# Kernel optimization log

Hardware: AMD Instinct MI355X
Metric: run time of the kernel (lower is better)

The kernel has to match this reference:

```python
import jax, jax.numpy as jnp
import numpy as np

B, T, D = 1, 2048, 1024
HQ, HKV, HD = 16, 4, 64
G = HQ // HKV
E, TOPK, F = 8, 2, 2752
LB = 0.01
SCALE = HD ** -0.5


def setup_inputs() -> dict:
    key = jax.random.key(0)
    ks = jax.random.split(key, 12)
    s = 0.02
    return {
        "x": jax.random.normal(ks[0], (B, T, D), jnp.float32),
        "g1": jnp.ones((D,), jnp.float32),
        "g2": jnp.ones((D,), jnp.float32),
        "wq": jax.random.normal(ks[1], (D, HQ * HD), jnp.float32) * s,
        "wk": jax.random.normal(ks[2], (D, HKV * HD), jnp.float32) * s,
        "wv": jax.random.normal(ks[3], (D, HKV * HD), jnp.float32) * s,
        "wo": jax.random.normal(ks[4], (D, D), jnp.float32) * s,
        "gate_w": jax.random.normal(ks[5], (D, E), jnp.float32) * s,
        "we_gate": jax.random.normal(ks[6], (E, D, F), jnp.float32) * s,
        "we_up": jax.random.normal(ks[7], (E, D, F), jnp.float32) * s,
        "we_down": jax.random.normal(ks[8], (E, F, D), jnp.float32) * s,
    }


def _rmsnorm(x, g, eps=1e-6):
    return x * g * jax.lax.rsqrt(jnp.mean(x * x, axis=-1, keepdims=True) + eps)


def _rope(q, k):
    # q: [B,HQ,T,HD], k: [B,HKV,T,HD]; standard rotate-half RoPE
    pos = jnp.arange(T, dtype=jnp.float32)
    inv_freq = 1.0 / (10000.0 ** (jnp.arange(0, HD, 2, dtype=jnp.float32) / HD))
    ang = pos[:, None] * inv_freq[None, :]                  # [T, HD/2]
    cos = jnp.concatenate([jnp.cos(ang), jnp.cos(ang)], -1)  # [T, HD]
    sin = jnp.concatenate([jnp.sin(ang), jnp.sin(ang)], -1)

    def rot_half(x):
        x1, x2 = jnp.split(x, 2, axis=-1)
        return jnp.concatenate([-x2, x1], axis=-1)

    def apply(x):
        return x * cos + rot_half(x) * sin
    return apply(q), apply(k)


def _attention(x, g1, wq, wk, wv, wo):
    h = _rmsnorm(x, g1)
    q = (h @ wq).reshape(B, T, HQ, HD).transpose(0, 2, 1, 3)   # [B,HQ,T,HD]
    k = (h @ wk).reshape(B, T, HKV, HD).transpose(0, 2, 1, 3)  # [B,HKV,T,HD]
    v = (h @ wv).reshape(B, T, HKV, HD).transpose(0, 2, 1, 3)
    q, k = _rope(q, k)
    qg = q.reshape(B, HKV, G, T, HD)
    # grouped scores without materializing repeated K/V
    scores = jnp.einsum('bkgtd,bksd->bkgts', qg, k) * SCALE     # [B,HKV,G,T,T]
    causal = jnp.tril(jnp.ones((T, T), bool))
    scores = jnp.where(causal, scores, jnp.float32(-jnp.inf))
    w = jax.nn.softmax(scores, axis=-1)
    o = jnp.einsum('bkgts,bksd->bkgtd', w, v)                  # [B,HKV,G,T,HD]
    o = o.reshape(B, HQ, T, HD).transpose(0, 2, 1, 3).reshape(B, T, D)
    return o @ wo


def _moe(x, g2, gate_w, we_gate, we_up, we_down):
    h = _rmsnorm(x, g2).reshape(B * T, D)                      # [N,D]
    N = B * T
    logits = h @ gate_w                                        # [N,E]
    probs = jax.nn.softmax(logits, axis=-1)
    topv, topi = jax.lax.top_k(probs, TOPK)                    # [N,TOPK]
    topv = topv / (topv.sum(-1, keepdims=True) + 1e-8)
    # dense combine weights [N,E]: same math as masked per-expert dispatch
    combine = jnp.zeros((N, E), h.dtype).at[jnp.arange(N)[:, None], topi].add(topv)
    gh = jnp.einsum('nd,edf->enf', h, we_gate)
    up = jnp.einsum('nd,edf->enf', h, we_up)
    y = jnp.einsum('enf,efd->end', jax.nn.silu(gh) * up, we_down)
    out = jnp.einsum('end,ne->nd', y, combine).reshape(B, T, D)
    # load-balancing aux loss
    frac = jnp.zeros((E,), probs.dtype).at[topi.reshape(-1)].add(1.0) / (N * TOPK)
    load = probs.mean(axis=0)
    aux = LB * E * jnp.sum(frac * load)
    return out, aux


def reference(x, g1, g2, wq, wk, wv, wo, gate_w, we_gate, we_up, we_down):
    x = x + _attention(x, g1, wq, wk, wv, wo)
    moe_out, aux = _moe(x, g2, gate_w, we_gate, we_up, we_down)
    x = x + moe_out
    return x, aux
```

## Files before the change

kernel.cpp:

```cpp
#include <hip/hip_runtime.h>
#include <cstdint>

typedef __attribute__((ext_vector_type(8))) short short8;
typedef __attribute__((ext_vector_type(4))) float floatx4;
typedef __attribute__((ext_vector_type(4))) unsigned short ushort4v;
typedef unsigned short ushort;

#define T_LEN 2048
#define D_DIM 1024
#define HQn 16
#define HKVn 4
#define NE 8
#define FF 2752
#define NTOK 2048
#define NSLOT 4096
#define ATT_SCALE 0.125f
#define GATE_TPB 16

__device__ inline ushort f2bf(float f) {
  union { float f; unsigned int i; } v; v.f = f;
  unsigned int r = v.i + 0x7fffu + ((v.i >> 16) & 1u);
  return (ushort)(r >> 16);
}
__device__ inline float bf2f(ushort h) {
  union { unsigned int i; float f; } v; v.i = ((unsigned int)h) << 16;
  return v.f;
}
__device__ inline void split8(const float* v, short8& hi, short8& lo) {
#pragma unroll
  for (int i = 0; i < 8; i++) {
    ushort h = f2bf(v[i]);
    hi[i] = (short)h;
    lo[i] = (short)f2bf(v[i] - bf2f(h));
  }
}
__device__ inline floatx4 mfma16(short8 a, short8 b, floatx4 c) {
  return __builtin_amdgcn_mfma_f32_16x16x32_bf16(a, b, c, 0, 0, 0);
}
#define DMA16(g, l)                                                              \
  __builtin_amdgcn_global_load_lds((const __attribute__((address_space(1))) void*)(g), \
                                   (__attribute__((address_space(3))) void*)(l), 16, 0, 0)

__global__ __launch_bounds__(256) void k_cvtT(const float* __restrict__ src,
                                              ushort* __restrict__ dst, int R, int C) {
  __shared__ float tile[32][33];
  size_t sb = (size_t)blockIdx.z * R * C;
  const float* s = src + sb;
  ushort* d = dst + sb;
  int r0 = blockIdx.y * 32, c0 = blockIdx.x * 32;
  int tc = threadIdx.x & 31, tr = threadIdx.x >> 5;
#pragma unroll
  for (int i = 0; i < 4; i++)
    tile[tr + i * 8][tc] = s[(size_t)(r0 + tr + i * 8) * C + c0 + tc];
  __syncthreads();
#pragma unroll
  for (int i = 0; i < 4; i++) {
    int cc = tr + i * 8;
    d[(size_t)(c0 + cc) * R + r0 + tc] = f2bf(tile[tc][cc]);
  }
}

__global__ __launch_bounds__(256) void k_cvtT2(const float* __restrict__ src,
                                               ushort* __restrict__ dh,
                                               ushort* __restrict__ dl, int R, int C) {
  __shared__ float tile[32][33];
  int r0 = blockIdx.y * 32, c0 = blockIdx.x * 32;
  int tc = threadIdx.x & 31, tr = threadIdx.x >> 5;
#pragma unroll
  for (int i = 0; i < 4; i++)
    tile[tr + i * 8][tc] = src[(size_t)(r0 + tr + i * 8) * C + c0 + tc];
  __syncthreads();
#pragma unroll
  for (int i = 0; i < 4; i++) {
    int cc = tr + i * 8;
    float v = tile[tc][cc];
    ushort h = f2bf(v);
    dh[(size_t)(c0 + cc) * R + r0 + tc] = h;
    dl[(size_t)(c0 + cc) * R + r0 + tc] = f2bf(v - bf2f(h));
  }
}

__global__ __launch_bounds__(256) void k_rmsnorm2(const float* __restrict__ x,
                                                  const float* __restrict__ g,
                                                  ushort* __restrict__ oh,
                                                  ushort* __restrict__ ol) {
  int row = blockIdx.x;
  int t = threadIdx.x;
  const float4* x4 = (const float4*)(x + (size_t)row * D_DIM);
  float4 v = x4[t];
  float ss = v.x * v.x + v.y * v.y + v.z * v.z + v.w * v.w;
#pragma unroll
  for (int off = 32; off; off >>= 1) ss += __shfl_xor(ss, off, 64);
  __shared__ float red[4];
  if ((t & 63) == 0) red[t >> 6] = ss;
  __syncthreads();
  float tot = red[0] + red[1] + red[2] + red[3];
  float sc = rsqrtf(tot * (1.0f / D_DIM) + 1e-6f);
  const float4* g4 = (const float4*)g;
  float4 gv = g4[t];
  float vals[4] = {v.x * gv.x * sc, v.y * gv.y * sc, v.z * gv.z * sc, v.w * gv.w * sc};
  ushort4v h4, l4;
#pragma unroll
  for (int i = 0; i < 4; i++) {
    ushort h = f2bf(vals[i]);
    h4[i] = h;
    l4[i] = f2bf(vals[i] - bf2f(h));
  }
  *(ushort4v*)(oh + (size_t)row * D_DIM + t * 4) = h4;
  *(ushort4v*)(ol + (size_t)row * D_DIM + t * 4) = l4;
}

__global__ __launch_bounds__(256) void k_sgemm(const ushort* __restrict__ Ahg,
                                               const ushort* __restrict__ Alg,
                                               const ushort* __restrict__ Bhg,
                                               const ushort* __restrict__ Blg,
                                               float* __restrict__ C,
                                               const float* __restrict__ res,
                                               int N, int K) {
  __shared__ __align__(16) ushort L0[12288], L1[12288];
  int tid = threadIdx.x;
  int m0 = blockIdx.y * 64, n0 = blockIdx.x * 128;
  int wave = tid >> 6, lane = tid & 63, quad = lane >> 4, l15 = lane & 15;
  int wm = (wave >> 1) * 32, wn = (wave & 1) * 64;
  floatx4 acc[2][4];
#pragma unroll
  for (int i = 0; i < 2; i++)
#pragma unroll
    for (int j = 0; j < 4; j++) acc[i][j] = (floatx4){0.f, 0.f, 0.f, 0.f};
  const ushort* src[6];
  int off[6];
  int srow = lane >> 2;
  int kc = ((lane & 3) ^ ((lane >> 3) & 3)) * 8;
#pragma unroll
  for (int j = 0; j < 6; j++) {
    int c = wave * 6 + j;
    if (c < 4) {
      src[j] = Ahg + (size_t)(m0 + c * 16 + srow) * K + kc;
      off[j] = c * 512;
    } else if (c < 8) {
      src[j] = Alg + (size_t)(m0 + (c - 4) * 16 + srow) * K + kc;
      off[j] = 2048 + (c - 4) * 512;
    } else if (c < 16) {
      src[j] = Bhg + (size_t)(n0 + (c - 8) * 16 + srow) * K + kc;
      off[j] = 4096 + (c - 8) * 512;
    } else {
      src[j] = Blg + (size_t)(n0 + (c - 16) * 16 + srow) * K + kc;
      off[j] = 8192 + (c - 16) * 512;
    }
  }
  auto stage = [&](ushort* Ld, int k0) {
#pragma unroll
    for (int j = 0; j < 6; j++) DMA16(src[j] + k0, Ld + off[j]);
  };
  auto compute = [&](const ushort* Ld) {
    const ushort* Ah = Ld;
    const ushort* Al = Ld + 2048;
    const ushort* Bh = Ld + 4096;
    const ushort* Bl = Ld + 8192;
    short8 ah[2], al[2], bh[4], bl[4];
#pragma unroll
    for (int mt = 0; mt < 2; mt++) {
      int ar = wm + mt * 16 + l15;
      int sw = (quad ^ ((ar >> 1) & 3)) * 8;
      ah[mt] = *(short8*)&Ah[ar * 32 + sw];
      al[mt] = *(short8*)&Al[ar * 32 + sw];
    }
#pragma unroll
    for (int nt = 0; nt < 4; nt++) {
      int br = wn + nt * 16 + l15;
      int sw = (quad ^ ((br >> 1) & 3)) * 8;
      bh[nt] = *(short8*)&Bh[br * 32 + sw];
      bl[nt] = *(short8*)&Bl[br * 32 + sw];
    }
#pragma unroll
    for (int mt = 0; mt < 2; mt++)
#pragma unroll
      for (int nt = 0; nt < 4; nt++) {
        acc[mt][nt] = mfma16(ah[mt], bh[nt], acc[mt][nt]);
        acc[mt][nt] = mfma16(ah[mt], bl[nt], acc[mt][nt]);
        acc[mt][nt] = mfma16(al[mt], bh[nt], acc[mt][nt]);
      }
  };
  int nt = K >> 5;
  stage(L0, 0);
  __syncthreads();
  for (int t = 0; t < nt; t++) {
    if ((t & 1) == 0) {
      if (t + 1 < nt) stage(L1, (t + 1) << 5);
      compute(L0);
    } else {
      if (t + 1 < nt) stage(L0, (t + 1) << 5);
      compute(L1);
    }
    __syncthreads();
  }
#pragma unroll
  for (int mt = 0; mt < 2; mt++) {
    int row = m0 + wm + mt * 16 + quad * 4;
#pragma unroll
    for (int nt2 = 0; nt2 < 4; nt2++) {
      int col = n0 + wn + nt2 * 16 + l15;
#pragma unroll
      for (int r = 0; r < 4; r++) {
        float v = acc[mt][nt2][r];
        if (res) v += res[(size_t)(row + r) * N + col];
        C[(size_t)(row + r) * N + col] = v;
      }
    }
  }
}

__global__ __launch_bounds__(256) void k_rope_cvt(const float* __restrict__ qkvf,
                                                  ushort* __restrict__ qhi,
                                                  ushort* __restrict__ qlo,
                                                  ushort* __restrict__ khi,
                                                  ushort* __restrict__ klo) {
  int t = blockIdx.x;
  const float* row = qkvf + (size_t)t * 1536;
  for (int it = threadIdx.x; it < (HQn + HKVn) * 32; it += 256) {
    int hh = it >> 5, i = it & 31;
    float inv = powf(10000.0f, -(float)i / 32.0f);
    float ang = (float)t * inv;
    float c = cosf(ang), s = sinf(ang);
    const float* p;
    ushort *dh, *dl;
    size_t base;
    if (hh < HQn) {
      p = row + hh * 64;
      base = ((size_t)hh * T_LEN + t) * 64;
      dh = qhi; dl = qlo;
    } else {
      int h2 = hh - HQn;
      p = row + 1024 + h2 * 64;
      base = ((size_t)h2 * T_LEN + t) * 64;
      dh = khi; dl = klo;
    }
    float a = p[i], b = p[i + 32];
    float v0 = a * c - b * s;
    float v1 = b * c + a * s;
    ushort h0 = f2bf(v0);
    dh[base + i] = h0;
    dl[base + i] = f2bf(v0 - bf2f(h0));
    ushort h1 = f2bf(v1);
    dh[base + i + 32] = h1;
    dl[base + i + 32] = f2bf(v1 - bf2f(h1));
  }
}

__global__ __launch_bounds__(256) void k_vT(const float* __restrict__ qkvf,
                                            ushort* __restrict__ vbth,
                                            ushort* __restrict__ vbtl) {
  __shared__ float tile[32][33];
  int t0 = blockIdx.x * 32;
  int dh = blockIdx.y;
  int col0 = 1280 + dh * 32;
  int tc = threadIdx.x & 31, tr = threadIdx.x >> 5;
#pragma unroll
  for (int i = 0; i < 4; i++)
    tile[tr + i * 8][tc] = qkvf[(size_t)(t0 + tr + i * 8) * 1536 + col0 + tc];
  __syncthreads();
#pragma unroll
  for (int i = 0; i < 4; i++) {
    int dd = tr + i * 8;
    float v = tile[tc][dd];
    ushort h = f2bf(v);
    size_t idx = (size_t)(dh * 32 + dd) * T_LEN + t0 + tc;
    vbth[idx] = h;
    vbtl[idx] = f2bf(v - bf2f(h));
  }
}

__global__ __launch_bounds__(256) void k_attn(const ushort* __restrict__ qhi,
                                              const ushort* __restrict__ qlo,
                                              const ushort* __restrict__ khi,
                                              const ushort* __restrict__ klo,
                                              const ushort* __restrict__ vbth,
                                              const ushort* __restrict__ vbtl,
                                              ushort* __restrict__ obh,
                                              ushort* __restrict__ obl) {
  __shared__ __align__(16) ushort Kh[4096], Kl[4096], Vh[4096], Vl[4096];
  __shared__ ushort Psh[4 * 16 * 72], Psl[4 * 16 * 72];
  int qh = blockIdx.y, kvh = qh >> 2;
  int tid = threadIdx.x, wave = tid >> 6, lane = tid & 63;
  int quad = lane >> 4, l15 = lane & 15;
  int sx = l15 >> 1;
  int rlb = lane >> 3;
  int csb = (lane & 7) ^ (lane >> 4);
#pragma unroll 1
  for (int hf = 0; hf < 2; hf++) {
    int xt = hf ? (31 - (int)blockIdx.x) : (int)blockIdx.x;
    int r0 = xt * 64;
    const ushort* qbh_ = qhi + ((size_t)qh * T_LEN + r0 + wave * 16 + l15) * 64;
    const ushort* qbl_ = qlo + ((size_t)qh * T_LEN + r0 + wave * 16 + l15) * 64;
    short8 aqh0 = *(const short8*)&qbh_[quad * 8];
    short8 aqh1 = *(const short8*)&qbh_[32 + quad * 8];
    short8 aql0 = *(const short8*)&qbl_[quad * 8];
    short8 aql1 = *(const short8*)&qbl_[32 + quad * 8];
    floatx4 oacc[4];
#pragma unroll
    for (int nt = 0; nt < 4; nt++) oacc[nt] = (floatx4){0.f, 0.f, 0.f, 0.f};
    float mrun[4], lrun[4];
#pragma unroll
    for (int r = 0; r < 4; r++) { mrun[r] = -INFINITY; lrun[r] = 0.f; }
    for (int cc = 0; cc <= xt; cc++) {
      __syncthreads();
      if (wave < 2) {
        const ushort* G = (wave == 0) ? khi : klo;
        ushort* L = (wave == 0) ? Kh : Kl;
        size_t rbase = (size_t)kvh * T_LEN + cc * 64;
#pragma unroll
        for (int i = 0; i < 8; i++) {
          int ch = csb ^ ((i & 1) * 4);
          DMA16(G + (rbase + i * 8 + rlb) * 64 + ch * 8, L + i * 512);
        }
      } else {
        const ushort* G = (wave == 2) ? vbth : vbtl;
        ushort* L = (wave == 2) ? Vh : Vl;
#pragma unroll
        for (int i = 0; i < 8; i++) {
          int ch = csb ^ ((i & 1) * 4);
          DMA16(G + ((size_t)(kvh * 64 + i * 8 + rlb)) * T_LEN + cc * 64 + ch * 8,
                L + i * 512);
        }
      }
      __syncthreads();
      floatx4 s[4];
#pragma unroll
      for (int nt = 0; nt < 4; nt++) {
        int row = nt * 16 + l15;
        short8 bh0 = *(short8*)&Kh[row * 64 + (quad ^ sx) * 8];
        short8 bh1 = *(short8*)&Kh[row * 64 + ((4 + quad) ^ sx) * 8];
        short8 bl0 = *(short8*)&Kl[row * 64 + (quad ^ sx) * 8];
        short8 bl1 = *(short8*)&Kl[row * 64 + ((4 + quad) ^ sx) * 8];
        floatx4 z = (floatx4){0.f, 0.f, 0.f, 0.f};
        z = mfma16(aqh0, bh0, z);
        z = mfma16(aqh1, bh1, z);
        z = mfma16(aqh0, bl0, z);
        z = mfma16(aqh1, bl1, z);
        z = mfma16(aql0, bh0, z);
        z = mfma16(aql1, bh1, z);
        s[nt] = z;
      }
      int rowg0 = r0 + wave * 16 + quad * 4;
#pragma unroll
      for (int nt = 0; nt < 4; nt++) {
        int colg = cc * 64 + nt * 16 + l15;
#pragma unroll
        for (int r = 0; r < 4; r++) {
          float v = s[nt][r] * ATT_SCALE;
          s[nt][r] = (colg > rowg0 + r) ? -INFINITY : v;
        }
      }
      float mnew[4], alpha[4], psum[4];
#pragma unroll
      for (int r = 0; r < 4; r++) {
        float mx = fmaxf(fmaxf(s[0][r], s[1][r]), fmaxf(s[2][r], s[3][r]));
#pragma unroll
        for (int off = 1; off < 16; off <<= 1) mx = fmaxf(mx, __shfl_xor(mx, off, 64));
        mnew[r] = fmaxf(mrun[r], mx);
        psum[r] = 0.f;
      }
#pragma unroll
      for (int nt = 0; nt < 4; nt++)
#pragma unroll
        for (int r = 0; r < 4; r++) {
          float p = __expf(s[nt][r] - mnew[r]);
          s[nt][r] = p;
          psum[r] += p;
        }
#pragma unroll
      for (int r = 0; r < 4; r++) {
        float ps = psum[r];
#pragma unroll
        for (int off = 1; off < 16; off <<= 1) ps += __shfl_xor(ps, off, 64);
        alpha[r] = __expf(mrun[r] - mnew[r]);
        lrun[r] = lrun[r] * alpha[r] + ps;
        mrun[r] = mnew[r];
      }
#pragma unroll
      for (int nt = 0; nt < 4; nt++)
#pragma unroll
        for (int r = 0; r < 4; r++) oacc[nt][r] *= alpha[r];
#pragma unroll
      for (int nt = 0; nt < 4; nt++)
#pragma unroll
        for (int r = 0; r < 4; r++) {
          float p = s[nt][r];
          ushort ph = f2bf(p);
          Psh[wave * 1152 + (quad * 4 + r) * 72 + nt * 16 + l15] = ph;
          Psl[wave * 1152 + (quad * 4 + r) * 72 + nt * 16 + l15] = f2bf(p - bf2f(ph));
        }
      short8 aph0 = *(short8*)&Psh[wave * 1152 + l15 * 72 + quad * 8];
      short8 aph1 = *(short8*)&Psh[wave * 1152 + l15 * 72 + 32 + quad * 8];
      short8 apl0 = *(short8*)&Psl[wave * 1152 + l15 * 72 + quad * 8];
      short8 apl1 = *(short8*)&Psl[wave * 1152 + l15 * 72 + 32 + quad * 8];
#pragma unroll
      for (int nt = 0; nt < 4; nt++) {
        int row = nt * 16 + l15;
        short8 bvh0 = *(short8*)&Vh[row * 64 + (quad ^ sx) * 8];
        short8 bvh1 = *(short8*)&Vh[row * 64 + ((4 + quad) ^ sx) * 8];
        short8 bvl0 = *(short8*)&Vl[row * 64 + (quad ^ sx) * 8];
        short8 bvl1 = *(short8*)&Vl[row * 64 + ((4 + quad) ^ sx) * 8];
        oacc[nt] = mfma16(aph0, bvh0, oacc[nt]);
        oacc[nt] = mfma16(aph1, bvh1, oacc[nt]);
        oacc[nt] = mfma16(aph0, bvl0, oacc[nt]);
        oacc[nt] = mfma16(aph1, bvl1, oacc[nt]);
        oacc[nt] = mfma16(apl0, bvh0, oacc[nt]);
        oacc[nt] = mfma16(apl1, bvh1, oacc[nt]);
      }
    }
#pragma unroll
    for (int nt = 0; nt < 4; nt++)
#pragma unroll
      for (int r = 0; r < 4; r++) {
        int rowg = r0 + wave * 16 + quad * 4 + r;
        float v = oacc[nt][r] / lrun[r];
        ushort h = f2bf(v);
        size_t idx = (size_t)rowg * D_DIM + qh * 64 + nt * 16 + l15;
        obh[idx] = h;
        obl[idx] = f2bf(v - bf2f(h));
      }
  }
}

__global__ __launch_bounds__(256) void k_gate(const float* __restrict__ x1,
                                              const float* __restrict__ g2,
                                              const float* __restrict__ gw,
                                              int* __restrict__ counts,
                                              int* __restrict__ ids,
                                              float* __restrict__ wts,
                                              float* __restrict__ load_sum) {
  __shared__ float lsum[NE];
  __shared__ int lcount[NE];
  __shared__ int lbase[NE];
  __shared__ int ltok[GATE_TPB * 2];
  __shared__ int lexp[GATE_TPB * 2];
  __shared__ float lwt[GATE_TPB * 2];
  int tid = threadIdx.x, wave = tid >> 6, lane = tid & 63;
  if (tid < NE) { lsum[tid] = 0.f; lcount[tid] = 0; }
  __syncthreads();
  int t0 = blockIdx.x * GATE_TPB;
#pragma unroll
  for (int tt = 0; tt < GATE_TPB / 4; tt++) {
    int tloc = tt * 4 + wave;
    int token = t0 + tloc;
    const float* xp = x1 + (size_t)token * D_DIM;
    float acc[NE] = {};
    float ss = 0.f;
    for (int d = lane; d < D_DIM; d += 64) {
      float xv = xp[d];
      ss += xv * xv;
      float hv = xv * g2[d];
#pragma unroll
      for (int e = 0; e < NE; e++) acc[e] += hv * gw[d * NE + e];
    }
#pragma unroll
    for (int off = 32; off; off >>= 1) ss += __shfl_xor(ss, off, 64);
#pragma unroll
    for (int e = 0; e < NE; e++)
#pragma unroll
      for (int off = 32; off; off >>= 1) acc[e] += __shfl_xor(acc[e], off, 64);
    if (lane == 0) {
      float sc = rsqrtf(ss * (1.0f / D_DIM) + 1e-6f);
      float mx = -1e30f;
#pragma unroll
      for (int e = 0; e < NE; e++) { acc[e] *= sc; mx = fmaxf(mx, acc[e]); }
      float p[NE], sum = 0.f;
#pragma unroll
      for (int e = 0; e < NE; e++) { p[e] = expf(acc[e] - mx); sum += p[e]; }
#pragma unroll
      for (int e = 0; e < NE; e++) p[e] /= sum;
      int i1 = 0;
#pragma unroll
      for (int e = 1; e < NE; e++) if (acc[e] > acc[i1]) i1 = e;
      int i2 = (i1 == 0) ? 1 : 0;
#pragma unroll
      for (int e = 0; e < NE; e++) if (e != i1 && acc[e] > acc[i2]) i2 = e;
      float denom = p[i1] + p[i2] + 1e-8f;
      int slot = tloc * 2;
      lexp[slot] = i1; ltok[slot] = token; lwt[slot] = p[i1] / denom;
      lexp[slot + 1] = i2; ltok[slot + 1] = token; lwt[slot + 1] = p[i2] / denom;
      atomicAdd(&lcount[i1], 1);
      atomicAdd(&lcount[i2], 1);
#pragma unroll
      for (int e = 0; e < NE; e++) atomicAdd(&lsum[e], p[e]);
    }
  }
  __syncthreads();
  if (tid < NE) {
    lbase[tid] = atomicAdd(&counts[tid], lcount[tid]);
    atomicAdd(&load_sum[tid], lsum[tid]);
    lcount[tid] = 0;
  }
  __syncthreads();
  if (tid < GATE_TPB * 2) {
    int e = lexp[tid];
    int off = atomicAdd(&lcount[e], 1);
    int pos = lbase[e] + off;
    ids[e * NTOK + pos] = ltok[tid];
    wts[e * NTOK + pos] = lwt[tid];
  }
}

__global__ void k_offsets(const int* __restrict__ counts, int* __restrict__ offsets) {
  if (threadIdx.x == 0 && blockIdx.x == 0) {
    int s = 0;
    for (int e = 0; e < NE; e++) { offsets[e] = s; s += counts[e]; }
  }
}

__global__ __launch_bounds__(256) void k_moe_gateup(const ushort* __restrict__ h,
                                                    const ushort* __restrict__ wgT,
                                                    const ushort* __restrict__ wuT,
                                                    const int* __restrict__ ids,
                                                    const float* __restrict__ wts,
                                                    const int* __restrict__ counts,
                                                    const int* __restrict__ offsets,
                                                    ushort* __restrict__ act) {
  int e = blockIdx.z;
  int cnt = counts[e];
  int m0 = blockIdx.y * 128;
  if (m0 >= cnt) return;
  int n0 = blockIdx.x * 64;
  __shared__ __align__(16) ushort L0[8192], L1[8192];
  __shared__ int toks[128];
  __shared__ float wrow[128];
  int tid = threadIdx.x;
  if (tid < 128) {
    int mm = m0 + tid;
    toks[tid] = (mm < cnt) ? ids[e * NTOK + mm] : 0;
    wrow[tid] = (mm < cnt) ? wts[e * NTOK + mm] : 0.f;
  }
  __syncthreads();
  int wave = tid >> 6, lane = tid & 63, quad = lane >> 4, l15 = lane & 15;
  int wm = (wave >> 1) * 64, wn = (wave & 1) * 32;
  const ushort* Wg = wgT + (size_t)e * FF * D_DIM;
  const ushort* Wu = wuT + (size_t)e * FF * D_DIM;
  const ushort* src[4];
  int off[4];
  int srow = lane >> 2;
  int kc = ((lane & 3) ^ ((lane >> 3) & 3)) * 8;
#pragma unroll
  for (int j = 0; j < 4; j++) {
    int c = wave * 4 + j;
    if (c < 8) {
      src[j] = h + (size_t)toks[c * 16 + srow] * D_DIM + kc;
      off[j] = c * 512;
    } else if (c < 12) {
      src[j] = Wg + (size_t)(n0 + (c - 8) * 16 + srow) * D_DIM + kc;
      off[j] = 4096 + (c - 8) * 512;
    } else {
      src[j] = Wu + (size_t)(n0 + (c - 12) * 16 + srow) * D_DIM + kc;
      off[j] = 6144 + (c - 12) * 512;
    }
  }
  floatx4 accg[4][2], accu[4][2];
#pragma unroll
  for (int i = 0; i < 4; i++)
#pragma unroll
    for (int j = 0; j < 2; j++) {
      accg[i][j] = (floatx4){0.f, 0.f, 0.f, 0.f};
      accu[i][j] = (floatx4){0.f, 0.f, 0.f, 0.f};
    }
  auto stage = [&](ushort* Ld, int k0) {
#pragma unroll
    for (int j = 0; j < 4; j++) DMA16(src[j] + k0, Ld + off[j]);
  };
  auto compute = [&](const ushort* Ld) {
    const ushort* As = Ld;
    const ushort* Bg = Ld + 4096;
    const ushort* Bu = Ld + 6144;
    short8 aF[4], bgF[2], buF[2];
#pragma unroll
    for (int mt = 0; mt < 4; mt++) {
      int ar = wm + mt * 16 + l15;
      int sw = (quad ^ ((ar >> 1) & 3)) * 8;
      aF[mt] = *(short8*)&As[ar * 32 + sw];
    }
#pragma unroll
    for (int nt = 0; nt < 2; nt++) {
      int br = wn + nt * 16 + l15;
      int sw = (quad ^ ((br >> 1) & 3)) * 8;
      bgF[nt] = *(short8*)&Bg[br * 32 + sw];
      buF[nt] = *(short8*)&Bu[br * 32 + sw];
    }
#pragma unroll
    for (int mt = 0; mt < 4; mt++)
#pragma unroll
      for (int nt = 0; nt < 2; nt++) {
        accg[mt][nt] = mfma16(aF[mt], bgF[nt], accg[mt][nt]);
        accu[mt][nt] = mfma16(aF[mt], buF[nt], accu[mt][nt]);
      }
  };
  stage(L0, 0);
  __syncthreads();
  for (int t = 0; t < 32; t++) {
    if ((t & 1) == 0) {
      if (t + 1 < 32) stage(L1, (t + 1) << 5);
      compute(L0);
    } else {
      if (t + 1 < 32) stage(L0, (t + 1) << 5);
      compute(L1);
    }
    __syncthreads();
  }
  int aoff = offsets[e];
#pragma unroll
  for (int mt = 0; mt < 4; mt++) {
    int mrow = wm + mt * 16 + quad * 4;
#pragma unroll
    for (int nt = 0; nt < 2; nt++) {
      int col = n0 + wn + nt * 16 + l15;
#pragma unroll
      for (int r = 0; r < 4; r++) {
        int ml = mrow + r;
        if (m0 + ml < cnt) {
          float g = accg[mt][nt][r];
          float u = accu[mt][nt][r];
          float sil = g / (1.f + __expf(-g));
          act[(size_t)(aoff + m0 + ml) * FF + col] = f2bf(sil * u * wrow[ml]);
        }
      }
    }
  }
}

__global__ __launch_bounds__(256) void k_moe_down(const ushort* __restrict__ act,
                                                  const ushort* __restrict__ wdT,
                                                  const int* __restrict__ ids,
                                                  const int* __restrict__ counts,
                                                  const int* __restrict__ offsets,
                                                  float* __restrict__ moe_acc) {
  int e = blockIdx.z & 7;
  int kh = blockIdx.z >> 3;
  int cnt = counts[e];
  int m0 = blockIdx.y * 128;
  if (m0 >= cnt) return;
  int n0 = blockIdx.x * 128;
  __shared__ __align__(16) ushort L0[8192], L1[8192];
  __shared__ int toks[128];
  int tid = threadIdx.x;
  if (tid < 128) {
    int mm = m0 + tid;
    toks[tid] = (mm < cnt) ? ids[e * NTOK + mm] : 0;
  }
  __syncthreads();
  int wave = tid >> 6, lane = tid & 63, quad = lane >> 4, l15 = lane & 15;
  int wm = (wave >> 1) * 64, wn = (wave & 1) * 64;
  int aoff = offsets[e];
  const ushort* Wd = wdT + (size_t)e * D_DIM * FF;
  const ushort* src[4];
  int off[4];
  int srow = lane >> 2;
  int kc = ((lane & 3) ^ ((lane >> 3) & 3)) * 8;
#pragma unroll
  for (int j = 0; j < 4; j++) {
    int c = wave * 4 + j;
    if (c < 8) {
      src[j] = act + (size_t)(aoff + m0 + c * 16 + srow) * FF + kc;
      off[j] = c * 512;
    } else {
      src[j] = Wd + (size_t)(n0 + (c - 8) * 16 + srow) * FF + kc;
      off[j] = 4096 + (c - 8) * 512;
    }
  }
  floatx4 acc[4][4];
#pragma unroll
  for (int i = 0; i < 4; i++)
#pragma unroll
    for (int j = 0; j < 4; j++) acc[i][j] = (floatx4){0.f, 0.f, 0.f, 0.f};
  auto stage = [&](ushort* Ld, int k0) {
#pragma unroll
    for (int j = 0; j < 4; j++) DMA16(src[j] + k0, Ld + off[j]);
  };
  auto compute = [&](const ushort* Ld) {
    const ushort* As = Ld;
    const ushort* Bs = Ld + 4096;
    short8 aF[4], bF[4];
#pragma unroll
    for (int mt = 0; mt < 4; mt++) {
      int ar = wm + mt * 16 + l15;
      int sw = (quad ^ ((ar >> 1) & 3)) * 8;
      aF[mt] = *(short8*)&As[ar * 32 + sw];
    }
#pragma unroll
    for (int nt = 0; nt < 4; nt++) {
      int br = wn + nt * 16 + l15;
      int sw = (quad ^ ((br >> 1) & 3)) * 8;
      bF[nt] = *(short8*)&Bs[br * 32 + sw];
    }
#pragma unroll
    for (int mt = 0; mt < 4; mt++)
#pragma unroll
      for (int nt = 0; nt < 4; nt++) acc[mt][nt] = mfma16(aF[mt], bF[nt], acc[mt][nt]);
  };
  int kbeg = kh * 1376;
  int nt = 43;
  stage(L0, kbeg);
  __syncthreads();
  for (int t = 0; t < nt; t++) {
    if ((t & 1) == 0) {
      if (t + 1 < nt) stage(L1, kbeg + ((t + 1) << 5));
      compute(L0);
    } else {
      if (t + 1 < nt) stage(L0, kbeg + ((t + 1) << 5));
      compute(L1);
    }
    __syncthreads();
  }
#pragma unroll
  for (int mt = 0; mt < 4; mt++) {
    int mrow = wm + mt * 16 + quad * 4;
#pragma unroll
    for (int nt2 = 0; nt2 < 4; nt2++) {
      int col = n0 + wn + nt2 * 16 + l15;
#pragma unroll
      for (int r = 0; r < 4; r++) {
        int ml = mrow + r;
        if (m0 + ml < cnt)
          atomicAdd(&moe_acc[(size_t)toks[ml] * D_DIM + col], acc[mt][nt2][r]);
      }
    }
  }
}

__global__ __launch_bounds__(256) void k_add(const float* __restrict__ a,
                                             const float* __restrict__ b,
                                             float* __restrict__ o) {
  int i = blockIdx.x * 256 + threadIdx.x;
  float4 va = ((const float4*)a)[i];
  float4 vb = ((const float4*)b)[i];
  float4 vo;
  vo.x = va.x + vb.x; vo.y = va.y + vb.y; vo.z = va.z + vb.z; vo.w = va.w + vb.w;
  ((float4*)o)[i] = vo;
}

__global__ void k_aux(const int* __restrict__ counts, const float* __restrict__ load_sum,
                      float* __restrict__ out_aux) {
  if (threadIdx.x == 0 && blockIdx.x == 0) {
    float s = 0.f;
    for (int e = 0; e < NE; e++)
      s += ((float)counts[e] / (float)NSLOT) * (load_sum[e] / (float)NTOK);
    *out_aux = 0.01f * (float)NE * s;
  }
}

extern "C" void kernel_launch(void* const* d_in, const int* in_sizes, int n_in,
                              void* d_out, int out_size, void* d_ws, size_t ws_size,
                              hipStream_t stream) {
  const float* x = (const float*)d_in[0];
  const float* g1 = (const float*)d_in[1];
  const float* g2 = (const float*)d_in[2];
  const float* wq = (const float*)d_in[3];
  const float* wk = (const float*)d_in[4];
  const float* wv = (const float*)d_in[5];
  const float* wo = (const float*)d_in[6];
  const float* gate_w = (const float*)d_in[7];
  const float* we_gate = (const float*)d_in[8];
  const float* we_up = (const float*)d_in[9];
  const float* we_down = (const float*)d_in[10];
  float* out = (float*)d_out;

  char* w = (char*)d_ws;
  size_t o = 0;
  auto alloc = [&](size_t bytes) -> char* {
    char* p = w + o;
    o = (o + bytes + 255) & ~(size_t)255;
    return p;
  };
  ushort* h1h = (ushort*)alloc((size_t)NTOK * D_DIM * 2);
  ushort* h1l = (ushort*)alloc((size_t)NTOK * D_DIM * 2);
  float* qkvf = (float*)alloc((size_t)NTOK * 1536 * 4);
  ushort* qhi = (ushort*)alloc((size_t)HQn * T_LEN * 64 * 2);
  ushort* qlo = (ushort*)alloc((size_t)HQn * T_LEN * 64 * 2);
  ushort* khi = (ushort*)alloc((size_t)HKVn * T_LEN * 64 * 2);
  ushort* klo = (ushort*)alloc((size_t)HKVn * T_LEN * 64 * 2);
  ushort* vbth = (ushort*)alloc((size_t)HKVn * 64 * T_LEN * 2);
  ushort* vbtl = (ushort*)alloc((size_t)HKVn * 64 * T_LEN * 2);
  ushort* obh = (ushort*)alloc((size_t)NTOK * D_DIM * 2);
  ushort* obl = (ushort*)alloc((size_t)NTOK * D_DIM * 2);
  float* x1 = (float*)alloc((size_t)NTOK * D_DIM * 4);
  float* moe_acc = (float*)alloc((size_t)NTOK * D_DIM * 4);
  ushort* act = (ushort*)alloc((size_t)(NSLOT + 128) * FF * 2);
  ushort* qkvwTh = (ushort*)alloc((size_t)1536 * 1024 * 2);
  ushort* qkvwTl = (ushort*)alloc((size_t)1536 * 1024 * 2);
  ushort* woTh = (ushort*)alloc((size_t)1024 * 1024 * 2);
  ushort* woTl = (ushort*)alloc((size_t)1024 * 1024 * 2);
  ushort* h2h = (ushort*)alloc((size_t)NTOK * D_DIM * 2);
  ushort* h2l = (ushort*)alloc((size_t)NTOK * D_DIM * 2);
  ushort* wgT = (ushort*)alloc((size_t)NE * FF * D_DIM * 2);
  ushort* wuT = (ushort*)alloc((size_t)NE * FF * D_DIM * 2);
  ushort* wdT = (ushort*)alloc((size_t)NE * D_DIM * FF * 2);
  int* counts = (int*)alloc(NE * 4);
  int* offsets = (int*)alloc(NE * 4);
  float* load_sum = (float*)alloc(NE * 4);
  int* ids = (int*)alloc((size_t)NE * NTOK * 4);
  float* wts = (float*)alloc((size_t)NE * NTOK * 4);

  hipMemsetAsync(moe_acc, 0, (size_t)NTOK * D_DIM * 4, stream);
  hipMemsetAsync(counts, 0, 768, stream);

  k_cvtT2<<<dim3(32, 32), 256, 0, stream>>>(wq, qkvwTh, qkvwTl, 1024, 1024);
  k_cvtT2<<<dim3(8, 32), 256, 0, stream>>>(wk, qkvwTh + (size_t)1024 * 1024,
                                           qkvwTl + (size_t)1024 * 1024, 1024, 256);
  k_cvtT2<<<dim3(8, 32), 256, 0, stream>>>(wv, qkvwTh + (size_t)1280 * 1024,
                                           qkvwTl + (size_t)1280 * 1024, 1024, 256);
  k_cvtT2<<<dim3(32, 32), 256, 0, stream>>>(wo, woTh, woTl, 1024, 1024);
  k_cvtT<<<dim3(86, 32, 8), 256, 0, stream>>>(we_gate, wgT, 1024, 2752);
  k_cvtT<<<dim3(86, 32, 8), 256, 0, stream>>>(we_up, wuT, 1024, 2752);
  k_cvtT<<<dim3(32, 86, 8), 256, 0, stream>>>(we_down, wdT, 2752, 1024);

  k_rmsnorm2<<<NTOK, 256, 0, stream>>>(x, g1, h1h, h1l);
  k_sgemm<<<dim3(12, 32), 256, 0, stream>>>(h1h, h1l, qkvwTh, qkvwTl, qkvf, nullptr,
                                            1536, 1024);
  k_rope_cvt<<<T_LEN, 256, 0, stream>>>(qkvf, qhi, qlo, khi, klo);
  k_vT<<<dim3(64, 8), 256, 0, stream>>>(qkvf, vbth, vbtl);
  k_attn<<<dim3(16, 16), 256, 0, stream>>>(qhi, qlo, khi, klo, vbth, vbtl, obh, obl);
  k_sgemm<<<dim3(8, 32), 256, 0, stream>>>(obh, obl, woTh, woTl, x1, x, 1024, 1024);

  k_rmsnorm2<<<NTOK, 256, 0, stream>>>(x1, g2, h2h, h2l);
  k_gate<<<NTOK / GATE_TPB, 256, 0, stream>>>(x1, g2, gate_w, counts, ids, wts, load_sum);
  k_offsets<<<1, 1, 0, stream>>>(counts, offsets);
  k_moe_gateup<<<dim3(43, 16, 8), 256, 0, stream>>>(h2h, wgT, wuT, ids, wts, counts,
                                                    offsets, act);
  k_moe_down<<<dim3(8, 16, 16), 256, 0, stream>>>(act, wdT, ids, counts, offsets, moe_acc);
  k_add<<<(NTOK * D_DIM) / (256 * 4), 256, 0, stream>>>(x1, moe_acc, out);
  k_aux<<<1, 1, 0, stream>>>(counts, load_sum, out + (size_t)NTOK * D_DIM);
}
```

Baseline: 710.9 us.

## Triple-buffer GEMM K-loop with vmcnt waits and a single barrier per tile

Replaces the double-buffered LDS staging in the split-bf16 GEMM, MoE gate/up and MoE down kernels with a three-buffer ring that prefetches two tiles ahead. Each iteration waits with an explicit s_waitcnt vmcnt on the older loads, then issues one raw s_barrier instead of a __syncthreads after compute. The aim is to hide more global-load latency and cut barrier overhead. The cost is 50% more shared memory per block, which may lower occupancy. The hand-written waitcnt counts must also match the number of loads per stage, and correctness relies on the direct-to-LDS load semantics.

Result: faster. 683.3 us (-3.9%).

```diff
diff --git a/kernel.cpp b/kernel.cpp
--- a/kernel.cpp
+++ b/kernel.cpp
@@ -17,6 +17,8 @@
 #define ATT_SCALE 0.125f
 #define GATE_TPB 16
 
+#define WAITCNT(N) asm volatile("s_waitcnt vmcnt(" #N ")" ::: "memory")
+
 __device__ inline ushort f2bf(float f) {
   union { float f; unsigned int i; } v; v.f = f;
   unsigned int r = v.i + 0x7fffu + ((v.i >> 16) & 1u);
@@ -117,7 +119,7 @@
                                                float* __restrict__ C,
                                                const float* __restrict__ res,
                                                int N, int K) {
-  __shared__ __align__(16) ushort L0[12288], L1[12288];
+  __shared__ __align__(16) ushort L[36864];
   int tid = threadIdx.x;
   int m0 = blockIdx.y * 64, n0 = blockIdx.x * 128;
   int wave = tid >> 6, lane = tid & 63, quad = lane >> 4, l15 = lane & 15;
@@ -181,18 +183,20 @@
         acc[mt][nt] = mfma16(al[mt], bh[nt], acc[mt][nt]);
       }
   };
-  int nt = K >> 5;
-  stage(L0, 0);
-  __syncthreads();
-  for (int t = 0; t < nt; t++) {
-    if ((t & 1) == 0) {
-      if (t + 1 < nt) stage(L1, (t + 1) << 5);
-      compute(L0);
-    } else {
-      if (t + 1 < nt) stage(L0, (t + 1) << 5);
-      compute(L1);
-    }
-    __syncthreads();
+  int ntile = K >> 5;
+  stage(L, 0);
+  stage(L + 12288, 32);
+  int cb = 0;
+  for (int t = 0; t < ntile; t++) {
+    if (t + 1 < ntile) { WAITCNT(6); } else { WAITCNT(0); }
+    __builtin_amdgcn_s_barrier();
+    __builtin_amdgcn_sched_barrier(0);
+    if (t + 2 < ntile) {
+      int sb = cb + 2; if (sb >= 3) sb -= 3;
+      stage(L + sb * 12288, (t + 2) << 5);
+    }
+    compute(L + cb * 12288);
+    if (++cb == 3) cb = 0;
   }
 #pragma unroll
   for (int mt = 0; mt < 2; mt++) {
@@ -522,7 +526,7 @@
   int m0 = blockIdx.y * 128;
   if (m0 >= cnt) return;
   int n0 = blockIdx.x * 64;
-  __shared__ __align__(16) ushort L0[8192], L1[8192];
+  __shared__ __align__(16) ushort L[24576];
   __shared__ int toks[128];
   __shared__ float wrow[128];
   int tid = threadIdx.x;
@@ -592,17 +596,19 @@
         accu[mt][nt] = mfma16(aF[mt], buF[nt], accu[mt][nt]);
       }
   };
-  stage(L0, 0);
-  __syncthreads();
+  stage(L, 0);
+  stage(L + 8192, 32);
+  int cb = 0;
   for (int t = 0; t < 32; t++) {
-    if ((t & 1) == 0) {
-      if (t + 1 < 32) stage(L1, (t + 1) << 5);
-      compute(L0);
-    } else {
-      if (t + 1 < 32) stage(L0, (t + 1) << 5);
-      compute(L1);
-    }
-    __syncthreads();
+    if (t + 1 < 32) { WAITCNT(4); } else { WAITCNT(0); }
+    __builtin_amdgcn_s_barrier();
+    __builtin_amdgcn_sched_barrier(0);
+    if (t + 2 < 32) {
+      int sb = cb + 2; if (sb >= 3) sb -= 3;
+      stage(L + sb * 8192, (t + 2) << 5);
+    }
+    compute(L + cb * 8192);
+    if (++cb == 3) cb = 0;
   }
   int aoff = offsets[e];
 #pragma unroll
@@ -637,7 +643,7 @@
   int m0 = blockIdx.y * 128;
   if (m0 >= cnt) return;
   int n0 = blockIdx.x * 128;
-  __shared__ __align__(16) ushort L0[8192], L1[8192];
+  __shared__ __align__(16) ushort L[24576];
   __shared__ int toks[128];
   int tid = threadIdx.x;
   if (tid < 128) {
@@ -695,18 +701,19 @@
       for (int nt = 0; nt < 4; nt++) acc[mt][nt] = mfma16(aF[mt], bF[nt], acc[mt][nt]);
   };
   int kbeg = kh * 1376;
-  int nt = 43;
-  stage(L0, kbeg);
-  __syncthreads();
-  for (int t = 0; t < nt; t++) {
-    if ((t & 1) == 0) {
-      if (t + 1 < nt) stage(L1, kbeg + ((t + 1) << 5));
-      compute(L0);
-    } else {
-      if (t + 1 < nt) stage(L0, kbeg + ((t + 1) << 5));
-      compute(L1);
-    }
-    __syncthreads();
+  stage(L, kbeg);
+  stage(L + 8192, kbeg + 32);
+  int cb = 0;
+  for (int t = 0; t < 43; t++) {
+    if (t + 1 < 43) { WAITCNT(4); } else { WAITCNT(0); }
+    __builtin_amdgcn_s_barrier();
+    __builtin_amdgcn_sched_barrier(0);
+    if (t + 2 < 43) {
+      int sb = cb + 2; if (sb >= 3) sb -= 3;
+      stage(L + sb * 8192, kbeg + ((t + 2) << 5));
+    }
+    compute(L + cb * 8192);
+    if (++cb == 3) cb = 0;
   }
 #pragma unroll
   for (int mt = 0; mt < 4; mt++) {
```
